# Optimization experiments

Measured on AMD Instinct MI355X. Metric: run time of the kernel, lower is better.

## Reference

```python
import jax, jax.numpy as jnp
import numpy as np

B, S, D, H = 2, 2048, 2048, 16
DH = D // H  # 128


def _rope_tables(seq_len, head_dim, base=10000.0):
    inv_freq = 1.0 / (base ** (jnp.arange(0, head_dim, 2, dtype=jnp.float32) / head_dim))
    t = jnp.arange(seq_len, dtype=jnp.float32)
    freqs = jnp.outer(t, inv_freq)                      # [S, DH/2]
    emb = jnp.concatenate([freqs, freqs], axis=-1)      # [S, DH]
    return jnp.cos(emb), jnp.sin(emb)


def _rotate_half(x):
    x1, x2 = jnp.split(x, 2, axis=-1)
    return jnp.concatenate([-x2, x1], axis=-1)


def setup_inputs() -> dict:
    key = jax.random.key(0)
    ks = jax.random.split(key, 5)
    sc = 0.02
    return {
        "hidden_states": jax.random.normal(ks[0], (B, S, D), jnp.float32),
        "Wq": jax.random.normal(ks[1], (D, D), jnp.float32) * sc,
        "Wk": jax.random.normal(ks[2], (D, D), jnp.float32) * sc,
        "Wv": jax.random.normal(ks[3], (D, D), jnp.float32) * sc,
        "Wo": jax.random.normal(ks[4], (D, D), jnp.float32) * sc,
        "medical_bias": jnp.zeros((1, H, 1, 1), jnp.float32),
    }


def reference(hidden_states, Wq, Wk, Wv, Wo, medical_bias):
    b, s, _ = hidden_states.shape
    # torch Linear: y = x @ W.T  (W is [out, in])
    def proj(x, W):
        y = jnp.einsum('bsd,ed->bse', x, W)
        return y.reshape(b, s, H, DH).transpose(0, 2, 1, 3)  # [b,H,s,DH]

    q = proj(hidden_states, Wq)
    k = proj(hidden_states, Wk)
    v = proj(hidden_states, Wv)

    cos, sin = _rope_tables(s, DH)                 # [s, DH]
    cos = cos[None, None]                          # [1,1,s,DH]
    sin = sin[None, None]
    q = q * cos + _rotate_half(q) * sin
    k = k * cos + _rotate_half(k) * sin

    scores = jnp.einsum('bhqd,bhkd->bhqk', q, k) / jnp.sqrt(jnp.float32(DH))
    scores = scores + medical_bias                 # learned per-head bias
    probs = jax.nn.softmax(scores, axis=-1)
    out = jnp.einsum('bhqk,bhkd->bhqd', probs, v)  # [b,H,s,DH]
    out = out.transpose(0, 2, 1, 3).reshape(b, s, D)
    return jnp.einsum('bsd,ed->bse', out, Wo)
```

## Files before the change

### kernel.cpp

```cpp
#include <hip/hip_runtime.h>
#include <hip/hip_bf16.h>
#include <stdint.h>


#define B_ 2
#define S_ 2048
#define D_ 2048
#define H_ 16

typedef float f32x4 __attribute__((ext_vector_type(4)));
typedef short s16x8 __attribute__((ext_vector_type(8)));

__device__ __forceinline__ unsigned short f2bf(float f) {
  union { float f; uint32_t u; } c; c.f = f;
  return (unsigned short)((c.u + 0x7fffu + ((c.u >> 16) & 1u)) >> 16);
}

__device__ __forceinline__ unsigned short bfc(float f) {
  __hip_bfloat16 h = __float2bfloat16(f);
  unsigned short u;
  __builtin_memcpy(&u, &h, 2);
  return u;
}

#define FAST_EXP2(x) __builtin_amdgcn_exp2f(x)

__device__ __forceinline__ void gld_lds16(const void* g, void* l) {
  __builtin_amdgcn_global_load_lds(
      (const __attribute__((address_space(1))) uint32_t*)g,
      (__attribute__((address_space(3))) uint32_t*)l, 16, 0, 0);
}

__global__ __launch_bounds__(256) void k_f2bf_all(
    const float* __restrict__ hs, const float* __restrict__ wq,
    const float* __restrict__ wk, const float* __restrict__ wv,
    const float* __restrict__ wo, unsigned short* __restrict__ hb,
    unsigned short* __restrict__ wall, float2* __restrict__ t2) {
  const int NH = 2097152, NW = 1048576;
  const int NF = NH + 4 * NW;
  const int NT = 131072;
  int i = blockIdx.x * 256 + threadIdx.x;
  const int stride = gridDim.x * 256;
  for (; i < NF + NT; i += stride) {
    if (i < NF) {
      f32x4 v;
      ushort4* dst;
      if (i < NH) {
        v = ((const f32x4*)hs)[i];
        dst = (ushort4*)hb + i;
      } else {
        const int j = i - NH;
        const int rgn = j >> 20;
        const int o = j & (NW - 1);
        const float* s = (rgn == 0) ? wq : (rgn == 1) ? wk : (rgn == 2) ? wv : wo;
        v = ((const f32x4*)s)[o];
        dst = (ushort4*)wall + j;
      }
      ushort4 u;
      u.x = f2bf(v.x); u.y = f2bf(v.y); u.z = f2bf(v.z); u.w = f2bf(v.w);
      *dst = u;
    } else {
      const int t = i - NF;
      const int s = t >> 6, j = t & 63;
      float inv = expf(-(float)j * (1.0f / 64.0f) * 9.210340371976184f);
      float sv, cv;
      sincosf((float)s * inv, &sv, &cv);
      t2[t] = float2{cv, sv};
    }
  }
}

__global__ __launch_bounds__(256, 2) void k_gemmq(
    const unsigned short* __restrict__ A,
    const unsigned short* __restrict__ W0,
    const unsigned short* __restrict__ W1,
    const unsigned short* __restrict__ W2,
    unsigned short* __restrict__ Qo,
    unsigned short* __restrict__ Ko,
    unsigned short* __restrict__ VT,
    const float2* __restrict__ tab) {
  __shared__ unsigned short Al[3][256 * 32];
  __shared__ unsigned short Bl[3][128 * 32];

  const int l0 = ((int)blockIdx.z * 16 + (int)blockIdx.y) * 16 + (int)blockIdx.x;
  const int wg = (l0 & 7) * 96 + (l0 >> 3);
  const int z = wg >> 8;
  const int ww = wg & 255;
  const int row0 = (ww >> 4) * 256;
  const int col0 = (ww & 15) * 128;
  const unsigned short* __restrict__ Wp = (z == 0) ? W0 : (z == 1) ? W1 : W2;

  const int tid = threadIdx.x;
  const int w = tid >> 6, l = tid & 63;
  const int c16 = l & 15, g = l >> 4;

  const int sr = w * 16 + (l >> 2);
  const int ssl = (l & 3) ^ ((l >> 3) & 3);
  const int scol = ssl << 3;

  const int swz = g ^ ((c16 >> 1) & 3);
  const int abase = (w * 64 + c16) * 64 + swz * 16;
  const int bbase = c16 * 64 + swz * 16;

  f32x4 acc[4][8];
#pragma unroll
  for (int m = 0; m < 4; ++m)
#pragma unroll
    for (int n = 0; n < 8; ++n)
      acc[m][n] = f32x4{0.f, 0.f, 0.f, 0.f};

#define STAGE_Q(K0, BUF)                                                       \
  do {                                                                         \
    _Pragma("unroll") for (int i = 0; i < 4; ++i)                              \
        gld_lds16(&A[(size_t)(row0 + i * 64 + sr) * 2048 + (K0) + scol],       \
                  &Al[BUF][(i * 64 + w * 16) * 32]);                           \
    _Pragma("unroll") for (int j = 0; j < 2; ++j)                              \
        gld_lds16(&Wp[(size_t)(col0 + j * 64 + sr) * 2048 + (K0) + scol],      \
                  &Bl[BUF][(j * 64 + w * 16) * 32]);                           \
  } while (0)

#define COMPUTE_Q(BUF)                                                         \
  do {                                                                         \
    const char* AB = (const char*)&Al[0][0] + (BUF)*16384;                     \
    const char* BB = (const char*)&Bl[0][0] + (BUF)*8192;                      \
    s16x8 a[4], b[8];                                                          \
    _Pragma("unroll") for (int m = 0; m < 4; ++m)                              \
        a[m] = *(const s16x8*)(AB + abase + m * 1024);                         \
    _Pragma("unroll") for (int n = 0; n < 8; ++n)                              \
        b[n] = *(const s16x8*)(BB + bbase + n * 1024);                         \
    __builtin_amdgcn_s_setprio(1);                                             \
    _Pragma("unroll") for (int m = 0; m < 4; ++m)                              \
        _Pragma("unroll") for (int n = 0; n < 8; ++n)                          \
            acc[m][n] = __builtin_amdgcn_mfma_f32_16x16x32_bf16(               \
                a[m], b[n], acc[m][n], 0, 0, 0);                               \
    __builtin_amdgcn_s_setprio(0);                                             \
  } while (0)

  STAGE_Q(0, 0);
  STAGE_Q(32, 1);
  int bcur = 0, bnxt = 2;
  for (int t = 0; t < 64; ++t) {
    if (t < 62) {
      STAGE_Q((t + 2) * 32, bnxt);
      asm volatile("s_waitcnt vmcnt(6)" ::: "memory");
    } else {
      asm volatile("s_waitcnt vmcnt(0)" ::: "memory");
    }
    asm volatile("s_barrier" ::: "memory");
    COMPUTE_Q(bcur);
    asm volatile("s_barrier" ::: "memory");
    bcur = (bcur == 2) ? 0 : bcur + 1;
    bnxt = (bnxt == 2) ? 0 : bnxt + 1;
  }
#undef STAGE_Q
#undef COMPUTE_Q

  if (z == 2) {
#pragma unroll
    for (int m = 0; m < 4; ++m) {
      const int gr = row0 + w * 64 + m * 16 + g * 4;
      const int b_ = gr >> 11, s_ = gr & 2047;
#pragma unroll
      for (int n = 0; n < 8; ++n) {
        const int gc = col0 + n * 16 + c16;
        ushort4 o;
        o.x = bfc(acc[m][n][0]);
        o.y = bfc(acc[m][n][1]);
        o.z = bfc(acc[m][n][2]);
        o.w = bfc(acc[m][n][3]);
        *(ushort4*)&VT[((size_t)(b_ * 2048 + gc)) * 2048 + s_] = o;
      }
    }
  } else {
    unsigned short* __restrict__ O = z ? Ko : Qo;
    const float sc = z ? 1.0f : (0.08838834764831845f * 1.4426950408889634f);
#pragma unroll
    for (int m = 0; m < 4; ++m) {
#pragma unroll
      for (int r = 0; r < 4; ++r) {
        const int gr = row0 + w * 64 + m * 16 + g * 4 + r;
        const int s_ = gr & 2047;
#pragma unroll
        for (int n = 0; n < 4; ++n) {
          const float2 f = tab[s_ * 64 + n * 16 + c16];
          const float x1 = acc[m][n][r], x2 = acc[m][n + 4][r];
          O[(size_t)gr * 2048 + col0 + n * 16 + c16] =
              bfc((x1 * f.x - x2 * f.y) * sc);
          O[(size_t)gr * 2048 + col0 + 64 + n * 16 + c16] =
              bfc((x2 * f.x + x1 * f.y) * sc);
        }
      }
    }
  }
}

__global__ __launch_bounds__(256, 2) void k_gemm(
    const unsigned short* __restrict__ A,
    const unsigned short* __restrict__ W0,
    float* __restrict__ C0) {
  __shared__ unsigned short Al[2][128 * 64];
  __shared__ unsigned short Bl[2][128 * 64];

  const int l0 = (int)blockIdx.y * 16 + (int)blockIdx.x;
  const int wg = (l0 & 7) * 64 + (l0 >> 3);

  const int tid = threadIdx.x;
  const int w = tid >> 6;
  const int l = tid & 63;
  const int row0 = ((wg >> 4) & 31) * 128;
  const int col0 = (wg & 15) * 128;

  const int c16 = l & 15, g = l >> 4;
  const int cx = c16 & 7;

  const int srow = l >> 3;
  const int scol = ((l & 7) ^ (l >> 3)) << 3;

  int kbase[2];
#pragma unroll
  for (int kk = 0; kk < 2; ++kk)
    kbase[kk] = c16 * 128 + (((kk * 4 + g) ^ cx) << 4);
  const char* AW0 = (const char*)&Al[0][0] + w * 4096;
  const char* AW1 = (const char*)&Al[1][0] + w * 4096;
  const char* BB0 = (const char*)&Bl[0][0];
  const char* BB1 = (const char*)&Bl[1][0];

  f32x4 acc[2][8];
#pragma unroll
  for (int m = 0; m < 2; ++m)
#pragma unroll
    for (int n = 0; n < 8; ++n)
      acc[m][n] = f32x4{0.f, 0.f, 0.f, 0.f};

#define STAGE_G(K0, BUF)                                                       \
  do {                                                                         \
    _Pragma("unroll") for (int i = 0; i < 4; ++i) {                            \
      const int jj = (w << 2) + i;                                             \
      gld_lds16(&A[(size_t)(row0 + (jj << 3) + srow) * 2048 + (K0) + scol],    \
                &Al[BUF][jj * 512]);                                           \
      gld_lds16(&W0[(size_t)(col0 + (jj << 3) + srow) * 2048 + (K0) + scol],   \
                &Bl[BUF][jj * 512]);                                           \
    }                                                                          \
  } while (0)

#define COMPUTE_G(AW, BBp)                                                     \
  do {                                                                         \
    _Pragma("unroll") for (int kk = 0; kk < 2; ++kk) {                         \
      s16x8 a[2], b[8];                                                        \
      _Pragma("unroll") for (int m = 0; m < 2; ++m)                            \
          a[m] = *(const s16x8*)((AW) + m * 2048 + kbase[kk]);                 \
      _Pragma("unroll") for (int n = 0; n < 8; ++n)                            \
          b[n] = *(const s16x8*)((BBp) + n * 2048 + kbase[kk]);                \
      __builtin_amdgcn_s_setprio(1);                                           \
      _Pragma("unroll") for (int m = 0; m < 2; ++m)                            \
          _Pragma("unroll") for (int n = 0; n < 8; ++n)                        \
              acc[m][n] = __builtin_amdgcn_mfma_f32_16x16x32_bf16(             \
                  a[m], b[n], acc[m][n], 0, 0, 0);                             \
      __builtin_amdgcn_s_setprio(0);                                           \
    }                                                                          \
  } while (0)

  STAGE_G(0, 0);
  __syncthreads();
  for (int k0 = 0; k0 < 2048; k0 += 128) {
    STAGE_G(k0 + 64, 1);
    COMPUTE_G(AW0, BB0);
    __syncthreads();
    if (k0 + 128 < 2048) STAGE_G(k0 + 128, 0);
    COMPUTE_G(AW1, BB1);
    __syncthreads();
  }
#undef STAGE_G
#undef COMPUTE_G

#pragma unroll
  for (int m = 0; m < 2; ++m) {
    const int gr = row0 + w * 32 + m * 16 + g * 4;
#pragma unroll
    for (int n = 0; n < 8; ++n) {
      const int gc = col0 + n * 16 + c16;
#pragma unroll
      for (int r = 0; r < 4; ++r)
        C0[(size_t)(gr + r) * 2048 + gc] = acc[m][n][r];
    }
  }
}

__global__ __launch_bounds__(256, 2) void k_attn(
    const unsigned short* __restrict__ Qb,
    const unsigned short* __restrict__ Kb,
    const unsigned short* __restrict__ Vt,
    unsigned short* __restrict__ Ob) {
  __shared__ unsigned short Kl[2][64 * 128];
  __shared__ unsigned short Vl[2][128 * 64];
  __shared__ unsigned short Pl[4][16 * 64];

  const int l0 = (int)blockIdx.y * 16 + (int)blockIdx.x;
  const int wg = (l0 & 7) * 64 + (l0 >> 3);
  const int bh = wg >> 4;
  const int b = bh >> 4, h = bh & 15;

  const int tid = threadIdx.x, w = tid >> 6, l = tid & 63;
  const int q0 = (wg & 15) * 128 + w * 32;
  const int g = l >> 4, c16 = l & 15;
  const int cx = c16 & 7;

  int kaddr[4], vaddr[2];
#pragma unroll
  for (int kc = 0; kc < 4; ++kc)
    kaddr[kc] = c16 * 256 + ((((kc * 4 + g) ^ cx)) << 4);
#pragma unroll
  for (int kc2 = 0; kc2 < 2; ++kc2)
    vaddr[kc2] = c16 * 128 + ((((kc2 * 4 + g) ^ cx)) << 4);
  const char* PW = (const char*)&Pl[w][0];

  s16x8 qf[2][4];
#pragma unroll
  for (int qq = 0; qq < 2; ++qq)
#pragma unroll
    for (int kc = 0; kc < 4; ++kc)
      qf[qq][kc] = *(const s16x8*)&Qb[(size_t)(b * 2048 + q0 + qq * 16 + c16) * 2048 +
                                      h * 128 + kc * 32 + g * 8];

  f32x4 oacc[2][8];
  float mrow[2][4], lrow[2][4];
#pragma unroll
  for (int qq = 0; qq < 2; ++qq) {
#pragma unroll
    for (int df = 0; df < 8; ++df) oacc[qq][df] = f32x4{0.f, 0.f, 0.f, 0.f};
#pragma unroll
    for (int r = 0; r < 4; ++r) { mrow[qq][r] = -INFINITY; lrow[qq][r] = 0.f; }
  }

#define STAGE(T, BUF)                                                          \
  do {                                                                         \
    _Pragma("unroll") for (int i = 0; i < 4; ++i) {                            \
      const int jj = (w << 2) + i;                                             \
      const int krow = jj * 4 + (l >> 4);                                      \
      const int kslot = (l & 15) ^ (krow & 7);                                 \
      gld_lds16(&Kb[(size_t)(b * 2048 + (T) + krow) * 2048 + h * 128 +        \
                    (kslot << 3)],                                             \
                &Kl[BUF][jj * 512]);                                           \
      const int vrow = jj * 8 + (l >> 3);                                      \
      const int vslot = (l & 7) ^ (vrow & 7);                                  \
      gld_lds16(&Vt[(size_t)(bh * 128 + vrow) * 2048 + (T) + (vslot << 3)],    \
                &Vl[BUF][jj * 512]);                                           \
    }                                                                          \
  } while (0)

#define COMPUTE(BUF_)                                                          \
  do {                                                                         \
    f32x4 sacc[2][4];                                                          \
    _Pragma("unroll") for (int qq = 0; qq < 2; ++qq)                           \
        _Pragma("unroll") for (int n = 0; n < 4; ++n)                          \
            sacc[qq][n] = f32x4{0.f, 0.f, 0.f, 0.f};                           \
    const char* KB = (const char*)&Kl[BUF_][0];                                \
    __builtin_amdgcn_s_setprio(1);                                             \
    _Pragma("unroll") for (int kc = 0; kc < 4; ++kc) {                         \
      s16x8 kb[4];                                                             \
      _Pragma("unroll") for (int n = 0; n < 4; ++n)                            \
          kb[n] = *(const s16x8*)(KB + kaddr[kc] + n * 4096);                  \
      _Pragma("unroll") for (int qq = 0; qq < 2; ++qq)                         \
          _Pragma("unroll") for (int n = 0; n < 4; ++n)                        \
              sacc[qq][n] = __builtin_amdgcn_mfma_f32_16x16x32_bf16(           \
                  qf[qq][kc], kb[n], sacc[qq][n], 0, 0, 0);                    \
    }                                                                          \
    __builtin_amdgcn_s_setprio(0);                                             \
    float mx4[2][4];                                                           \
    float need = 0.f;                                                          \
    _Pragma("unroll") for (int qq = 0; qq < 2; ++qq)                           \
        _Pragma("unroll") for (int r = 0; r < 4; ++r) {                        \
      mx4[qq][r] = fmaxf(fmaxf(sacc[qq][0][r], sacc[qq][1][r]),                \
                         fmaxf(sacc[qq][2][r], sacc[qq][3][r]));               \
      need = fmaxf(need, mx4[qq][r] - mrow[qq][r]);                            \
    }                                                                          \
    if (!__all(need <= 8.0f)) {          \
      _Pragma("unroll") for (int qq = 0; qq < 2; ++qq)                         \
          _Pragma("unroll") for (int r = 0; r < 4; ++r) {                      \
        float mx = mx4[qq][r];                                                 \
        mx = fmaxf(mx, __shfl_xor(mx, 1));                                     \
        mx = fmaxf(mx, __shfl_xor(mx, 2));                                     \
        mx = fmaxf(mx, __shfl_xor(mx, 4));                                     \
        mx = fmaxf(mx, __shfl_xor(mx, 8));                                     \
        float mnew = fmaxf(mrow[qq][r], mx);                                   \
        float alpha = FAST_EXP2(mrow[qq][r] - mnew);                           \
        mrow[qq][r] = mnew;                                                    \
        lrow[qq][r] *= alpha;                                                  \
        _Pragma("unroll") for (int df = 0; df < 8; ++df)                       \
            oacc[qq][df][r] *= alpha;                                          \
      }                                                                        \
    }                                                                          \
    const char* VB = (const char*)&Vl[BUF_][0];                                \
    _Pragma("unroll") for (int qq = 0; qq < 2; ++qq) {                         \
      _Pragma("unroll") for (int r = 0; r < 4; ++r) {                          \
        float rs = 0.f;                                                        \
        _Pragma("unroll") for (int n = 0; n < 4; ++n) {                        \
          float p = FAST_EXP2(sacc[qq][n][r] - mrow[qq][r]);                   \
          sacc[qq][n][r] = p;                                                  \
          rs += p;                                                             \
        }                                                                      \
        lrow[qq][r] += rs;                                                     \
      }                                                                        \
      _Pragma("unroll") for (int n = 0; n < 4; ++n)                            \
          _Pragma("unroll") for (int r = 0; r < 4; ++r) {                      \
        const int prow = g * 4 + r;                                            \
        const int psl = (n * 2 + (c16 >> 3)) ^ (prow & 7);                     \
        Pl[w][prow * 64 + (psl << 3) + (c16 & 7)] = bfc(sacc[qq][n][r]);       \
      }                                                                        \
      __builtin_amdgcn_s_setprio(1);                                           \
      _Pragma("unroll") for (int kc2 = 0; kc2 < 2; ++kc2) {                    \
        s16x8 pa = *(const s16x8*)(PW + vaddr[kc2]);                           \
        _Pragma("unroll") for (int df = 0; df < 8; ++df) {                     \
          s16x8 vb = *(const s16x8*)(VB + vaddr[kc2] + df * 2048);             \
          oacc[qq][df] = __builtin_amdgcn_mfma_f32_16x16x32_bf16(              \
              pa, vb, oacc[qq][df], 0, 0, 0);                                  \
        }                                                                      \
      }                                                                        \
      __builtin_amdgcn_s_setprio(0);                                           \
    }                                                                          \
  } while (0)

  STAGE(0, 0);
  __syncthreads();
  for (int t = 0; t < 2048; t += 128) {
    STAGE(t + 64, 1);
    COMPUTE(0);
    __syncthreads();
    if (t + 128 < 2048) STAGE(t + 128, 0);
    COMPUTE(1);
    __syncthreads();
  }
#undef STAGE
#undef COMPUTE

#pragma unroll
  for (int qq = 0; qq < 2; ++qq)
#pragma unroll
    for (int r = 0; r < 4; ++r) {
      float tot = lrow[qq][r];
      tot += __shfl_xor(tot, 1);
      tot += __shfl_xor(tot, 2);
      tot += __shfl_xor(tot, 4);
      tot += __shfl_xor(tot, 8);
      const float inv = 1.0f / tot;
      const int srow_ = q0 + qq * 16 + g * 4 + r;
#pragma unroll
      for (int df = 0; df < 8; ++df)
        Ob[(size_t)(b * 2048 + srow_) * 2048 + h * 128 + df * 16 + c16] =
            bfc(oacc[qq][df][r] * inv);
    }
}

extern "C" void kernel_launch(void* const* d_in, const int* in_sizes, int n_in,
                              void* d_out, int out_size, void* d_ws, size_t ws_size,
                              hipStream_t stream) {
  const float* hs = (const float*)d_in[0];
  const float* Wq = (const float*)d_in[1];
  const float* Wk = (const float*)d_in[2];
  const float* Wv = (const float*)d_in[3];
  const float* Wo = (const float*)d_in[4];
  float* out = (float*)d_out;
  char* ws = (char*)d_ws;

  unsigned short* hb   = (unsigned short*)(ws + 0);
  unsigned short* wall = (unsigned short*)(ws + 16777216);
  unsigned short* wqb  = wall;
  unsigned short* wkb  = wall + 4194304;
  unsigned short* wvb  = wall + 8388608;
  unsigned short* wob  = wall + 12582912;
  unsigned short* Qbb  = (unsigned short*)(ws + 50331648);
  unsigned short* Kbb  = (unsigned short*)(ws + 67108864);
  unsigned short* Vt   = (unsigned short*)(ws + 83886080);
  float2*         tab2 = (float2*)(ws + 100663296);
  unsigned short* Ob   = hb;

  k_f2bf_all<<<2048, 256, 0, stream>>>(hs, Wq, Wk, Wv, Wo, hb, wall, tab2);

  k_gemmq<<<dim3(16, 16, 3), 256, 0, stream>>>(hb, wqb, wkb, wvb, Qbb, Kbb, Vt,
                                               tab2);
  k_attn<<<dim3(16, 32), 256, 0, stream>>>(Qbb, Kbb, Vt, Ob);
  k_gemm<<<dim3(16, 32), 256, 0, stream>>>(Ob, wob, out);
}
```

Baseline: 280.6 us.

## Switch QKV GEMM to double-buffered LDS with higher occupancy target

```diff
diff --git a/kernel.cpp b/kernel.cpp
--- a/kernel.cpp
+++ b/kernel.cpp
@@ -70,7 +70,7 @@
   }
 }
 
-__global__ __launch_bounds__(256, 2) void k_gemmq(
+__global__ __launch_bounds__(256, 3) void k_gemmq(
     const unsigned short* __restrict__ A,
     const unsigned short* __restrict__ W0,
     const unsigned short* __restrict__ W1,
@@ -79,8 +79,8 @@
     unsigned short* __restrict__ Ko,
     unsigned short* __restrict__ VT,
     const float2* __restrict__ tab) {
-  __shared__ unsigned short Al[3][256 * 32];
-  __shared__ unsigned short Bl[3][128 * 32];
+  __shared__ unsigned short Al[2][256 * 32];
+  __shared__ unsigned short Bl[2][128 * 32];
 
   const int l0 = ((int)blockIdx.z * 16 + (int)blockIdx.y) * 16 + (int)blockIdx.x;
   const int wg = (l0 & 7) * 96 + (l0 >> 3);
@@ -95,8 +95,7 @@
   const int c16 = l & 15, g = l >> 4;
 
   const int sr = w * 16 + (l >> 2);
-  const int ssl = (l & 3) ^ ((l >> 3) & 3);
-  const int scol = ssl << 3;
+  const int scol = ((l & 3) ^ ((l >> 3) & 3)) << 3;
 
   const int swz = g ^ ((c16 >> 1) & 3);
   const int abase = (w * 64 + c16) * 64 + swz * 16;
@@ -121,36 +120,30 @@
 
 #define COMPUTE_Q(BUF)                                                         \
   do {                                                                         \
-    const char* AB = (const char*)&Al[0][0] + (BUF)*16384;                     \
-    const char* BB = (const char*)&Bl[0][0] + (BUF)*8192;                      \
-    s16x8 a[4], b[8];                                                          \
+    const char* AB = (const char*)&Al[BUF][0];                                 \
+    const char* BB = (const char*)&Bl[BUF][0];                                 \
+    s16x8 a[4];                                                                \
     _Pragma("unroll") for (int m = 0; m < 4; ++m)                              \
         a[m] = *(const s16x8*)(AB + abase + m * 1024);                         \
-    _Pragma("unroll") for (int n = 0; n < 8; ++n)                              \
-        b[n] = *(const s16x8*)(BB + bbase + n * 1024);                         \
     __builtin_amdgcn_s_setprio(1);                                             \
-    _Pragma("unroll") for (int m = 0; m < 4; ++m)                              \
-        _Pragma("unroll") for (int n = 0; n < 8; ++n)                          \
-            acc[m][n] = __builtin_amdgcn_mfma_f32_16x16x32_bf16(               \
-                a[m], b[n], acc[m][n], 0, 0, 0);                               \
+    _Pragma("unroll") for (int n = 0; n < 8; ++n) {                            \
+      s16x8 b = *(const s16x8*)(BB + bbase + n * 1024);                        \
+      _Pragma("unroll") for (int m = 0; m < 4; ++m)                            \
+          acc[m][n] = __builtin_amdgcn_mfma_f32_16x16x32_bf16(                 \
+              a[m], b, acc[m][n], 0, 0, 0);                                    \
+    }                                                                          \
     __builtin_amdgcn_s_setprio(0);                                             \
   } while (0)
 
   STAGE_Q(0, 0);
-  STAGE_Q(32, 1);
-  int bcur = 0, bnxt = 2;
-  for (int t = 0; t < 64; ++t) {
-    if (t < 62) {
-      STAGE_Q((t + 2) * 32, bnxt);
-      asm volatile("s_waitcnt vmcnt(6)" ::: "memory");
-    } else {
-      asm volatile("s_waitcnt vmcnt(0)" ::: "memory");
-    }
-    asm volatile("s_barrier" ::: "memory");
-    COMPUTE_Q(bcur);
-    asm volatile("s_barrier" ::: "memory");
-    bcur = (bcur == 2) ? 0 : bcur + 1;
-    bnxt = (bnxt == 2) ? 0 : bnxt + 1;
+  __syncthreads();
+  for (int k0 = 0; k0 < 2048; k0 += 64) {
+    STAGE_Q(k0 + 32, 1);
+    COMPUTE_Q(0);
+    __syncthreads();
+    if (k0 + 64 < 2048) STAGE_Q(k0 + 64, 0);
+    COMPUTE_Q(1);
+    __syncthreads();
   }
 #undef STAGE_Q
 #undef COMPUTE_Q
@@ -366,6 +359,7 @@
                   qf[qq][kc], kb[n], sacc[qq][n], 0, 0, 0);                    \
     }                                                                          \
     __builtin_amdgcn_s_setprio(0);                                             \
+            \
     float mx4[2][4];                                                           \
     float need = 0.f;                                                          \
     _Pragma("unroll") for (int qq = 0; qq < 2; ++qq)                           \
@@ -391,6 +385,8 @@
       }                                                                        \
     }                                                                          \
     const char* VB = (const char*)&Vl[BUF_][0];                                \
+       \
+      \
     _Pragma("unroll") for (int qq = 0; qq < 2; ++qq) {                         \
       _Pragma("unroll") for (int r = 0; r < 4; ++r) {                          \
         float rs = 0.f;                                                        \
```

Result: faster. 273.4 us (-2.5%).
